# Kernel tuning notes

Hardware: AMD Instinct MI355X
Metric: run time of the kernel (lower is better)

The kernel has to match this reference:

```python
import jax, jax.numpy as jnp
import numpy as np

B, T = 32, 1024
AC, SE, H, NH = 20, 16, 64, 4
HD = H // NH  # 16


def setup_inputs() -> dict:
    key = jax.random.key(0)
    ks = jax.random.split(key, 8)
    g = 0.1  # xavier gain used in _init_weights (rough scale)
    return {
        'acoustic': jax.random.normal(ks[0], (B, T, AC), jnp.float32),
        'semantic': jax.random.normal(ks[1], (B, T, SE), jnp.float32),
        'Wq': jax.random.normal(ks[2], (H, SE), jnp.float32) * g,
        'bq': jnp.zeros((H,), jnp.float32),
        'Wkv': jax.random.normal(ks[3], (2 * H, AC), jnp.float32) * g,
        'bkv': jnp.zeros((2 * H,), jnp.float32),
        'in_w': jax.random.normal(ks[4], (3 * H, H), jnp.float32) * g,
        'in_b': jnp.zeros((3 * H,), jnp.float32),
        'out_w': jax.random.normal(ks[5], (H, H), jnp.float32) * g,
        'out_b': jnp.zeros((H,), jnp.float32),
        'proj_w': jax.random.normal(ks[6], (AC, H), jnp.float32) * g,
        'proj_b': jnp.zeros((AC,), jnp.float32),
        'residual_logit': jnp.float32(-2.0),
        'ln_gamma': jnp.ones((AC,), jnp.float32),
        'ln_beta': jnp.zeros((AC,), jnp.float32),
    }


def _std(x, axis, keepdims=True):
    # torch.std default: unbiased (ddof=1)
    return jnp.std(x, axis=axis, ddof=1, keepdims=keepdims)


def reference(acoustic, semantic, Wq, bq, Wkv, bkv, in_w, in_b, out_w, out_b,
              proj_w, proj_b, residual_logit, ln_gamma, ln_beta):
    # projections to hidden space
    q = semantic @ Wq.T + bq                       # [B,T,H]
    kv = acoustic @ Wkv.T + bkv                    # [B,T,2H]
    k, v = kv[..., :H], kv[..., H:]
    # nn.MultiheadAttention in-projection
    qi = q @ in_w[:H].T + in_b[:H]
    ki = k @ in_w[H:2 * H].T + in_b[H:2 * H]
    vi = v @ in_w[2 * H:].T + in_b[2 * H:]
    # split heads -> [B,T,NH,HD]
    qh = qi.reshape(B, T, NH, HD)
    kh = ki.reshape(B, T, NH, HD)
    vh = vi.reshape(B, T, NH, HD)
    scores = jnp.einsum('bqhd,bkhd->bhqk', qh, kh) / jnp.sqrt(jnp.float32(HD))
    attn = jax.nn.softmax(scores, axis=-1)         # [B,NH,T,T]
    ctx = jnp.einsum('bhqk,bkhd->bqhd', attn, vh).reshape(B, T, H)
    attended = ctx @ out_w.T + out_b               # MHA out_proj
    enhanced_raw = attended @ proj_w.T + proj_b    # [B,T,AC]
    enhanced = acoustic + jax.nn.sigmoid(residual_logit) * enhanced_raw

    # statistics over batch+time (no_grad in torch -> stop_gradient)
    orig_mean = jax.lax.stop_gradient(jnp.mean(acoustic, axis=(0, 1), keepdims=True))
    orig_std = jax.lax.stop_gradient(_std(acoustic, (0, 1)) + 1e-8)
    a_n = (acoustic - orig_mean) / orig_std
    e_n = (enhanced - orig_mean) / orig_std
    std_ratio = _std(e_n, (0, 1)) / (_std(a_n, (0, 1)) + 1e-8)
    std_corr = jnp.where(std_ratio < 0.4, 0.4 / std_ratio, jnp.ones_like(std_ratio))
    enhanced_final = (e_n * std_corr) * orig_std + orig_mean

    # LayerNorm over last dim (biased variance, eps=1e-5)
    mu = jnp.mean(enhanced_final, axis=-1, keepdims=True)
    var = jnp.mean(jnp.square(enhanced_final - mu), axis=-1, keepdims=True)
    return (enhanced_final - mu) * jax.lax.rsqrt(var + 1e-5) * ln_gamma + ln_beta
```

## Files before the change

kernel.cpp:

```cpp
#include <hip/hip_runtime.h>
#include <hip/hip_bf16.h>
#include <math.h>

#define B 32
#define T 1024
#define AC 20
#define SE 16
#define H 64
#define NH 4
#define HD 16
#define NROW (B*T)
#define BH (B*NH)
#define NCHUNK (T/32)
#define NSLOT 128

typedef unsigned short u16;
typedef short short8 __attribute__((ext_vector_type(8)));
typedef float f32x16 __attribute__((ext_vector_type(16)));
typedef unsigned int uintx4 __attribute__((ext_vector_type(4)));

#define F_QB   (BH*T*16/2)
#define OFF_QB   0
#define OFF_KB   (OFF_QB + F_QB)
#define OFF_VT   (OFF_KB + F_QB)
#define OFF_CT   (OFF_VT + F_QB)
#define OFF_ET   (OFF_CT + H*NROW)
#define OFF_WF   (OFF_ET + AC*NROW)
#define OFF_ACC  (OFF_WF + 5120)
#define OFF_ST   (OFF_ACC + NSLOT*80)

#define WF_WQ 0
#define WF_BQ 1024
#define WF_WK 1088
#define WF_BK 2368
#define WF_WV 2432
#define WF_BV 3712
#define WF_WO 3776
#define WF_BO 5056
#define WF_TOTAL 5076

__device__ __forceinline__ u16 bf16b(float a) {
    __hip_bfloat16 t = __float2bfloat16(a);
    u16 u; __builtin_memcpy(&u, &t, 2); return u;
}
__device__ __forceinline__ unsigned packbf(float a, float b) {
    return (unsigned)bf16b(a) | ((unsigned)bf16b(b) << 16);
}

__global__ __launch_bounds__(256) void k_fuse(
    const float* __restrict__ Wq, const float* __restrict__ bq,
    const float* __restrict__ Wkv, const float* __restrict__ bkv,
    const float* __restrict__ in_w, const float* __restrict__ in_b,
    const float* __restrict__ out_w, const float* __restrict__ out_b,
    const float* __restrict__ proj_w, const float* __restrict__ proj_b,
    float* __restrict__ wf, float* __restrict__ accum) {
    int idx = blockIdx.x * 256 + threadIdx.x;
    if (idx < NSLOT*40) {
        accum[idx] = 0.f;
        accum[idx + NSLOT*40] = 0.f;
    }
    if (idx >= WF_TOTAL) return;
    if (idx < WF_BQ) {
        int i = idx >> 4, j = idx & 15;
        float s = 0.f;
        for (int m = 0; m < H; ++m) s += in_w[i*H + m] * Wq[m*SE + j];
        wf[idx] = 0.25f * s;
    } else if (idx < WF_WK) {
        int i = idx - WF_BQ;
        float s = in_b[i];
        for (int m = 0; m < H; ++m) s += in_w[i*H + m] * bq[m];
        wf[idx] = 0.25f * s;
    } else if (idx < WF_BK) {
        int r = idx - WF_WK; int i = r / AC, j = r % AC;
        float s = 0.f;
        for (int m = 0; m < H; ++m) s += in_w[(H+i)*H + m] * Wkv[m*AC + j];
        wf[idx] = s;
    } else if (idx < WF_WV) {
        int i = idx - WF_BK;
        float s = in_b[H + i];
        for (int m = 0; m < H; ++m) s += in_w[(H+i)*H + m] * bkv[m];
        wf[idx] = s;
    } else if (idx < WF_BV) {
        int r = idx - WF_WV; int i = r / AC, j = r % AC;
        float s = 0.f;
        for (int m = 0; m < H; ++m) s += in_w[(2*H+i)*H + m] * Wkv[(H+m)*AC + j];
        wf[idx] = s;
    } else if (idx < WF_WO) {
        int i = idx - WF_BV;
        float s = in_b[2*H + i];
        for (int m = 0; m < H; ++m) s += in_w[(2*H+i)*H + m] * bkv[H + m];
        wf[idx] = s;
    } else if (idx < WF_BO) {
        int r = idx - WF_WO; int c = r >> 6, d = r & 63;
        float s = 0.f;
        for (int m = 0; m < H; ++m) s += proj_w[c*H + m] * out_w[m*H + d];
        wf[idx] = s;
    } else {
        int c = idx - WF_BO;
        float s = proj_b[c];
        for (int m = 0; m < H; ++m) s += proj_w[c*H + m] * out_b[m];
        wf[idx] = s;
    }
}

__global__ __launch_bounds__(192) void k_qkv(
    const float* __restrict__ sem, const float* __restrict__ acst,
    const float* __restrict__ wf,
    u16* __restrict__ Qb, u16* __restrict__ Kb, u16* __restrict__ Vtb) {
    const int tid = threadIdx.x;
    const int sec = tid >> 4, r = tid & 15;
    const int row = blockIdx.x * 16 + r;
    const int b = row >> 10, t = row & 1023;
    const int type = sec >> 2, h = sec & 3;
    float o[16];
    if (type == 0) {
        float s[SE];
        const float4* sp = (const float4*)(sem + (size_t)row * SE);
        #pragma unroll
        for (int i = 0; i < 4; ++i) {
            float4 v = sp[i];
            s[4*i] = v.x; s[4*i+1] = v.y; s[4*i+2] = v.z; s[4*i+3] = v.w;
        }
        const float* wq = wf + WF_WQ + h*16*SE;
        const float* bq = wf + WF_BQ + h*16;
        #pragma unroll
        for (int ii = 0; ii < 16; ++ii) {
            float acc = bq[ii];
            #pragma unroll
            for (int j = 0; j < 4; ++j) {
                float4 w4 = *(const float4*)(wq + ii*SE + 4*j);
                acc += s[4*j]*w4.x + s[4*j+1]*w4.y + s[4*j+2]*w4.z + s[4*j+3]*w4.w;
            }
            o[ii] = acc;
        }
        unsigned* dst = (unsigned*)(Qb + (((size_t)(b*NH + h))*T + t)*16);
        #pragma unroll
        for (int i = 0; i < 8; ++i) dst[i] = packbf(o[2*i], o[2*i+1]);
    } else {
        float a[AC];
        const float4* ap = (const float4*)(acst + (size_t)row * AC);
        #pragma unroll
        for (int i = 0; i < 5; ++i) {
            float4 v = ap[i];
            a[4*i] = v.x; a[4*i+1] = v.y; a[4*i+2] = v.z; a[4*i+3] = v.w;
        }
        const float* wb = wf + (type == 1 ? WF_WK : WF_WV) + h*16*AC;
        const float* bb = wf + (type == 1 ? WF_BK : WF_BV) + h*16;
        #pragma unroll
        for (int ii = 0; ii < 16; ++ii) {
            float acc = bb[ii];
            #pragma unroll
            for (int j = 0; j < 5; ++j) {
                float4 w4 = *(const float4*)(wb + ii*AC + 4*j);
                acc += a[4*j]*w4.x + a[4*j+1]*w4.y + a[4*j+2]*w4.z + a[4*j+3]*w4.w;
            }
            o[ii] = acc;
        }
        if (type == 1) {
            unsigned* dst = (unsigned*)(Kb + (((size_t)(b*NH + h))*T + t)*16);
            #pragma unroll
            for (int i = 0; i < 8; ++i) dst[i] = packbf(o[2*i], o[2*i+1]);
        } else {
            u16* dst = Vtb + ((size_t)(b*NH + h)*64 + (t >> 4))*256 + (t & 15);
            #pragma unroll
            for (int d = 0; d < HD; ++d) dst[d*16] = bf16b(o[d]);
        }
    }
}

__global__ __launch_bounds__(256, 4) void k_attn(
    const u16* __restrict__ Qb, const u16* __restrict__ Kb, const u16* __restrict__ Vtb,
    float* __restrict__ ctxT) {
    const int tid  = threadIdx.x;
    const int lane = tid & 63;
    const int wv   = tid >> 6;
    const int blk  = blockIdx.x;
    const int bh   = blk & 127;
    const int qblk = blk >> 7;
    const int b = bh >> 2, h = bh & 3;
    const int l31 = lane & 31, hi2 = lane >> 5, l15 = lane & 15;
    const int q0 = qblk*128 + wv*32;

    const short8 qf = *(const short8*)(Qb + ((size_t)bh*T + q0 + l31)*16 + 8*hi2);
    const u16* kp = Kb + ((size_t)bh*T + l31)*16 + 8*hi2;
    const u16* vp = Vtb + (size_t)bh*16384 + l15*16 + 8*hi2;

    f32x16 acc = {0.f,0.f,0.f,0.f,0.f,0.f,0.f,0.f,0.f,0.f,0.f,0.f,0.f,0.f,0.f,0.f};
    const f32x16 z16 = {0.f,0.f,0.f,0.f,0.f,0.f,0.f,0.f,0.f,0.f,0.f,0.f,0.f,0.f,0.f,0.f};
    float ls = 0.f;

    short8 kf = *(const short8*)kp;
    short8 va = *(const short8*)vp;
    short8 vb = *(const short8*)(vp + 256);
    #pragma unroll 4
    for (int ch = 0; ch < NCHUNK; ++ch) {
        const int nx = (ch < NCHUNK-1) ? ch + 1 : ch;
        short8 kf_n = *(const short8*)(kp + (size_t)nx*512);
        short8 va_n = *(const short8*)(vp + (size_t)nx*512);
        short8 vb_n = *(const short8*)(vp + (size_t)nx*512 + 256);

        f32x16 sc = __builtin_amdgcn_mfma_f32_32x32x16_bf16(kf, qf, z16, 0, 0, 0);
        float p[16];
        #pragma unroll
        for (int r = 0; r < 16; ++r) p[r] = __expf(sc[r]);
        #pragma unroll
        for (int r = 0; r < 16; ++r) ls += p[r];

        unsigned u0 = packbf(p[0],  p[1]);
        unsigned u1 = packbf(p[2],  p[3]);
        unsigned u2 = packbf(p[4],  p[5]);
        unsigned u3 = packbf(p[6],  p[7]);
        unsigned u4 = packbf(p[8],  p[9]);
        unsigned u5 = packbf(p[10], p[11]);
        unsigned u6 = packbf(p[12], p[13]);
        unsigned u7 = packbf(p[14], p[15]);
        asm("v_permlane32_swap_b32 %0, %1" : "+v"(u2), "+v"(u0));
        asm("v_permlane32_swap_b32 %0, %1" : "+v"(u3), "+v"(u1));
        asm("v_permlane32_swap_b32 %0, %1" : "+v"(u6), "+v"(u4));
        asm("v_permlane32_swap_b32 %0, %1" : "+v"(u7), "+v"(u5));
        uintx4 t1 = {u0, u1, u2, u3};
        uintx4 t2 = {u4, u5, u6, u7};
        short8 pf1 = __builtin_bit_cast(short8, t1);
        short8 pf2 = __builtin_bit_cast(short8, t2);

        acc = __builtin_amdgcn_mfma_f32_32x32x16_bf16(va, pf1, acc, 0, 0, 0);
        acc = __builtin_amdgcn_mfma_f32_32x32x16_bf16(vb, pf2, acc, 0, 0, 0);

        kf = kf_n; va = va_n; vb = vb_n;
    }

    ls += __shfl_xor(ls, 32);
    const float inv = 1.f / ls;
    const int row = b*T + q0 + l31;
    #pragma unroll
    for (int r = 0; r < 8; ++r) {
        const int d = (r & 3) + 8*(r >> 2) + 4*hi2;
        ctxT[(size_t)(h*16 + d)*NROW + row] = acc[r] * inv;
    }
}

#define CSTR 65
__global__ __launch_bounds__(256) void k_proj(
    const float* __restrict__ ctxT, const float* __restrict__ acst,
    const float* __restrict__ wf, const float* __restrict__ rlogit,
    float* __restrict__ enhT, float* __restrict__ accum) {
    __shared__ float ctxs[64*CSTR];
    __shared__ __align__(16) float wsm[AC*H + AC];
    const int tid = threadIdx.x;
    for (int i = tid; i < AC*H + AC; i += 256) wsm[i] = wf[WF_WO + i];
    const int row0 = blockIdx.x * 64;
    for (int i = tid; i < 64*64; i += 256) {
        int ch = i >> 6, rr = i & 63;
        ctxs[rr*CSTR + ch] = ctxT[(size_t)ch*NROW + row0 + rr];
    }
    __syncthreads();
    const int r = tid & 63, cg = tid >> 6;
    const int row = row0 + r;
    float* slot = accum + (size_t)(blockIdx.x & (NSLOT-1)) * 80;
    float c64[H];
    #pragma unroll
    for (int k = 0; k < H; ++k) c64[k] = ctxs[r*CSTR + k];
    float sg = 1.f / (1.f + __expf(-rlogit[0]));
    #pragma unroll
    for (int j = 0; j < 5; ++j) {
        int ch = cg*5 + j;
        float s = wsm[AC*H + ch];
        const float4* w4 = (const float4*)(wsm + ch*H);
        #pragma unroll
        for (int k = 0; k < 16; ++k) {
            float4 w = w4[k];
            s += c64[4*k]*w.x + c64[4*k+1]*w.y + c64[4*k+2]*w.z + c64[4*k+3]*w.w;
        }
        float a = acst[(size_t)row*AC + ch];
        float e = a + sg * s;
        enhT[(size_t)ch * NROW + row] = e;
        float sa = a, qa = a*a, se = e, qe = e*e;
        #pragma unroll
        for (int m = 1; m <= 32; m <<= 1) {
            sa += __shfl_xor(sa, m); qa += __shfl_xor(qa, m);
            se += __shfl_xor(se, m); qe += __shfl_xor(qe, m);
        }
        if (r == 0) {
            atomicAdd(&slot[ch*4+0], sa);
            atomicAdd(&slot[ch*4+1], qa);
            atomicAdd(&slot[ch*4+2], se);
            atomicAdd(&slot[ch*4+3], qe);
        }
    }
}

__global__ __launch_bounds__(640) void k_stats2(
    const float* __restrict__ accum, float* __restrict__ stats) {
    __shared__ float red[80*8];
    __shared__ float acs[80];
    const int tx = threadIdx.x;
    const int c = tx >> 3, p = tx & 7;
    float s0 = 0.f, s1 = 0.f, s2 = 0.f, s3 = 0.f;
    #pragma unroll
    for (int i = 0; i < 4; ++i) {
        int sl = p + (4*i)*8;
        s0 += accum[(size_t)sl*80 + c];
        s1 += accum[(size_t)(sl+8)*80 + c];
        s2 += accum[(size_t)(sl+16)*80 + c];
        s3 += accum[(size_t)(sl+24)*80 + c];
    }
    red[c*8 + p] = (s0 + s1) + (s2 + s3);
    __syncthreads();
    if (tx < 80) {
        float t = 0.f;
        #pragma unroll
        for (int i = 0; i < 8; ++i) t += red[tx*8 + i];
        acs[tx] = t;
    }
    __syncthreads();
    if (tx < AC) {
        const float Nf = (float)NROW;
        float sa = acs[tx*4+0], qa = acs[tx*4+1];
        float se = acs[tx*4+2], qe = acs[tx*4+3];
        float mu  = sa / Nf;
        float va  = (qa - sa*sa/Nf) / (Nf - 1.f);
        float sda = sqrtf(fmaxf(va, 0.f));
        float osd = sda + 1e-8f;
        float ve  = (qe - se*se/Nf) / (Nf - 1.f);
        float sde = sqrtf(fmaxf(ve, 0.f));
        float ratio = (sde / osd) / (sda / osd + 1e-8f);
        float corr  = (ratio < 0.4f) ? (0.4f / ratio) : 1.f;
        stats[tx*2]   = mu;
        stats[tx*2+1] = corr;
    }
}

__global__ __launch_bounds__(128) void k_final(
    const float* __restrict__ enhT, const float* __restrict__ stats,
    const float* __restrict__ gamma, const float* __restrict__ beta,
    float* __restrict__ out) {
    __shared__ float acs[40];
    const int tx = threadIdx.x;
    if (tx < 40) acs[tx] = stats[tx];
    __syncthreads();
    int row = blockIdx.x * 128 + tx;
    float ef[AC];
    #pragma unroll
    for (int c = 0; c < AC; ++c) {
        float mu = acs[c*2], corr = acs[c*2+1];
        float e = enhT[(size_t)c * NROW + row];
        ef[c] = (e - mu) * corr + mu;
    }
    float m = 0.f;
    #pragma unroll
    for (int c = 0; c < AC; ++c) m += ef[c];
    m *= (1.f / AC);
    float v = 0.f;
    #pragma unroll
    for (int c = 0; c < AC; ++c) { float d = ef[c] - m; v += d*d; }
    v *= (1.f / AC);
    float inv = rsqrtf(v + 1e-5f);
    float o[AC];
    #pragma unroll
    for (int c = 0; c < AC; ++c) o[c] = (ef[c] - m) * inv * gamma[c] + beta[c];
    float4* op = (float4*)(out + (size_t)row * AC);
    #pragma unroll
    for (int i = 0; i < 5; ++i)
        op[i] = make_float4(o[4*i], o[4*i+1], o[4*i+2], o[4*i+3]);
}

extern "C" void kernel_launch(void* const* d_in, const int* in_sizes, int n_in,
                              void* d_out, int out_size, void* d_ws, size_t ws_size,
                              hipStream_t stream) {
    (void)in_sizes; (void)n_in; (void)out_size; (void)ws_size;
    const float* acoustic = (const float*)d_in[0];
    const float* semantic = (const float*)d_in[1];
    const float* Wq     = (const float*)d_in[2];
    const float* bq     = (const float*)d_in[3];
    const float* Wkv    = (const float*)d_in[4];
    const float* bkv    = (const float*)d_in[5];
    const float* in_w   = (const float*)d_in[6];
    const float* in_b   = (const float*)d_in[7];
    const float* out_w  = (const float*)d_in[8];
    const float* out_b  = (const float*)d_in[9];
    const float* proj_w = (const float*)d_in[10];
    const float* proj_b = (const float*)d_in[11];
    const float* rlogit = (const float*)d_in[12];
    const float* gamma  = (const float*)d_in[13];
    const float* beta   = (const float*)d_in[14];
    float* ws = (float*)d_ws;
    u16* Qb  = (u16*)(ws + OFF_QB);
    u16* Kb  = (u16*)(ws + OFF_KB);
    u16* Vtb = (u16*)(ws + OFF_VT);
    float* ctxT  = ws + OFF_CT;
    float* enhT  = ws + OFF_ET;
    float* wf    = ws + OFF_WF;
    float* accum = ws + OFF_ACC;
    float* stats = ws + OFF_ST;
    float* out = (float*)d_out;

    k_fuse<<<(WF_TOTAL + 255)/256, 256, 0, stream>>>(Wq, bq, Wkv, bkv, in_w, in_b,
                                                     out_w, out_b, proj_w, proj_b, wf, accum);
    k_qkv<<<NROW/16, 192, 0, stream>>>(semantic, acoustic, wf, Qb, Kb, Vtb);
    k_attn<<<8*BH, 256, 0, stream>>>(Qb, Kb, Vtb, ctxT);
    k_proj<<<NROW/64, 256, 0, stream>>>(ctxT, acoustic, wf, rlogit, enhT, accum);
    k_stats2<<<1, 640, 0, stream>>>(accum, stats);
    k_final<<<NROW/128, 128, 0, stream>>>(enhT, stats, gamma, beta, out);
}
```

Baseline: 159.3 us.

## Fuse output projection and statistics into attention kernel, drop ctx buffer

The attention kernel's block mapping changes so each block covers all four heads of one batch for 32 query rows, with one wave per head. The per-head context goes into shared memory, and the same block then applies the fused out/proj weights, the residual sigmoid blend and the per-channel sum/sumsq atomics. This removes the separate k_proj launch and the global round trip of the 64-channel ctxT buffer. In exchange each block does serial projection work after its attention loop, adds about 13 KB of shared memory per block, and has fewer query rows per head per block.

Result: faster. 151.7 us (-4.8%).

```diff
diff --git a/kernel.cpp b/kernel.cpp
--- a/kernel.cpp
+++ b/kernel.cpp
@@ -23,8 +23,7 @@
 #define OFF_QB   0
 #define OFF_KB   (OFF_QB + F_QB)
 #define OFF_VT   (OFF_KB + F_QB)
-#define OFF_CT   (OFF_VT + F_QB)
-#define OFF_ET   (OFF_CT + H*NROW)
+#define OFF_ET   (OFF_VT + F_QB)
 #define OFF_WF   (OFF_ET + AC*NROW)
 #define OFF_ACC  (OFF_WF + 5120)
 #define OFF_ST   (OFF_ACC + NSLOT*80)
@@ -168,18 +167,24 @@
     }
 }
 
+#define CSTR 66
 __global__ __launch_bounds__(256, 4) void k_attn(
     const u16* __restrict__ Qb, const u16* __restrict__ Kb, const u16* __restrict__ Vtb,
-    float* __restrict__ ctxT) {
+    const float* __restrict__ acst, const float* __restrict__ wf,
+    const float* __restrict__ rlogit,
+    float* __restrict__ enhT, float* __restrict__ accum) {
+    __shared__ __align__(16) float ctxs[32*CSTR];
+    __shared__ __align__(16) float wsm[AC*H + AC];
     const int tid  = threadIdx.x;
     const int lane = tid & 63;
     const int wv   = tid >> 6;
+    for (int i = tid; i < AC*H + AC; i += 256) wsm[i] = wf[WF_WO + i];
     const int blk  = blockIdx.x;
-    const int bh   = blk & 127;
-    const int qblk = blk >> 7;
-    const int b = bh >> 2, h = bh & 3;
+    const int b    = blk & 31;
+    const int qblk = blk >> 5;
     const int l31 = lane & 31, hi2 = lane >> 5, l15 = lane & 15;
-    const int q0 = qblk*128 + wv*32;
+    const int bh = b*NH + wv;
+    const int q0 = qblk*32;
 
     const short8 qf = *(const short8*)(Qb + ((size_t)bh*T + q0 + l31)*16 + 8*hi2);
     const u16* kp = Kb + ((size_t)bh*T + l31)*16 + 8*hi2;
@@ -231,56 +236,47 @@
 
     ls += __shfl_xor(ls, 32);
     const float inv = 1.f / ls;
-    const int row = b*T + q0 + l31;
     #pragma unroll
     for (int r = 0; r < 8; ++r) {
         const int d = (r & 3) + 8*(r >> 2) + 4*hi2;
-        ctxT[(size_t)(h*16 + d)*NROW + row] = acc[r] * inv;
-    }
-}
-
-#define CSTR 65
-__global__ __launch_bounds__(256) void k_proj(
-    const float* __restrict__ ctxT, const float* __restrict__ acst,
-    const float* __restrict__ wf, const float* __restrict__ rlogit,
-    float* __restrict__ enhT, float* __restrict__ accum) {
-    __shared__ float ctxs[64*CSTR];
-    __shared__ __align__(16) float wsm[AC*H + AC];
-    const int tid = threadIdx.x;
-    for (int i = tid; i < AC*H + AC; i += 256) wsm[i] = wf[WF_WO + i];
-    const int row0 = blockIdx.x * 64;
-    for (int i = tid; i < 64*64; i += 256) {
-        int ch = i >> 6, rr = i & 63;
-        ctxs[rr*CSTR + ch] = ctxT[(size_t)ch*NROW + row0 + rr];
+        ctxs[l31*CSTR + wv*16 + d] = acc[r] * inv;
     }
     __syncthreads();
-    const int r = tid & 63, cg = tid >> 6;
-    const int row = row0 + r;
-    float* slot = accum + (size_t)(blockIdx.x & (NSLOT-1)) * 80;
-    float c64[H];
-    #pragma unroll
-    for (int k = 0; k < H; ++k) c64[k] = ctxs[r*CSTR + k];
-    float sg = 1.f / (1.f + __expf(-rlogit[0]));
-    #pragma unroll
-    for (int j = 0; j < 5; ++j) {
-        int ch = cg*5 + j;
+
+    const int rq = tid & 31, g = tid >> 5;
+    const int row = b*T + q0 + rq;
+    const float sg = 1.f / (1.f + __expf(-rlogit[0]));
+    float* slot = accum + (size_t)(blk & (NSLOT-1)) * 80;
+    const int nj = (g < 4) ? 3 : 2;
+    for (int j = 0; j < nj; ++j) {
+        const int ch = g + 8*j;
         float s = wsm[AC*H + ch];
-        const float4* w4 = (const float4*)(wsm + ch*H);
-        #pragma unroll
-        for (int k = 0; k < 16; ++k) {
-            float4 w = w4[k];
-            s += c64[4*k]*w.x + c64[4*k+1]*w.y + c64[4*k+2]*w.z + c64[4*k+3]*w.w;
-        }
-        float a = acst[(size_t)row*AC + ch];
-        float e = a + sg * s;
+        #pragma unroll
+        for (int kc = 0; kc < 4; ++kc) {
+            float c0 = ctxs[rq*CSTR + kc*16 +  0], c1 = ctxs[rq*CSTR + kc*16 +  1];
+            float c2 = ctxs[rq*CSTR + kc*16 +  2], c3 = ctxs[rq*CSTR + kc*16 +  3];
+            float c4 = ctxs[rq*CSTR + kc*16 +  4], c5 = ctxs[rq*CSTR + kc*16 +  5];
+            float c6 = ctxs[rq*CSTR + kc*16 +  6], c7 = ctxs[rq*CSTR + kc*16 +  7];
+            float c8 = ctxs[rq*CSTR + kc*16 +  8], c9 = ctxs[rq*CSTR + kc*16 +  9];
+            float cA = ctxs[rq*CSTR + kc*16 + 10], cB = ctxs[rq*CSTR + kc*16 + 11];
+            float cC = ctxs[rq*CSTR + kc*16 + 12], cD = ctxs[rq*CSTR + kc*16 + 13];
+            float cE = ctxs[rq*CSTR + kc*16 + 14], cF = ctxs[rq*CSTR + kc*16 + 15];
+            const float* w = wsm + ch*H + kc*16;
+            s += c0*w[0] + c1*w[1] + c2*w[2] + c3*w[3]
+               + c4*w[4] + c5*w[5] + c6*w[6] + c7*w[7]
+               + c8*w[8] + c9*w[9] + cA*w[10] + cB*w[11]
+               + cC*w[12] + cD*w[13] + cE*w[14] + cF*w[15];
+        }
+        const float a = acst[(size_t)row*AC + ch];
+        const float e = a + sg * s;
         enhT[(size_t)ch * NROW + row] = e;
         float sa = a, qa = a*a, se = e, qe = e*e;
         #pragma unroll
-        for (int m = 1; m <= 32; m <<= 1) {
+        for (int m = 1; m <= 16; m <<= 1) {
             sa += __shfl_xor(sa, m); qa += __shfl_xor(qa, m);
             se += __shfl_xor(se, m); qe += __shfl_xor(qe, m);
         }
-        if (r == 0) {
+        if (rq == 0) {
             atomicAdd(&slot[ch*4+0], sa);
             atomicAdd(&slot[ch*4+1], qa);
             atomicAdd(&slot[ch*4+2], se);
@@ -387,7 +383,6 @@
     u16* Qb  = (u16*)(ws + OFF_QB);
     u16* Kb  = (u16*)(ws + OFF_KB);
     u16* Vtb = (u16*)(ws + OFF_VT);
-    float* ctxT  = ws + OFF_CT;
     float* enhT  = ws + OFF_ET;
     float* wf    = ws + OFF_WF;
     float* accum = ws + OFF_ACC;
@@ -397,8 +392,7 @@
     k_fuse<<<(WF_TOTAL + 255)/256, 256, 0, stream>>>(Wq, bq, Wkv, bkv, in_w, in_b,
                                                      out_w, out_b, proj_w, proj_b, wf, accum);
     k_qkv<<<NROW/16, 192, 0, stream>>>(semantic, acoustic, wf, Qb, Kb, Vtb);
-    k_attn<<<8*BH, 256, 0, stream>>>(Qb, Kb, Vtb, ctxT);
-    k_proj<<<NROW/64, 256, 0, stream>>>(ctxT, acoustic, wf, rlogit, enhT, accum);
+    k_attn<<<1024, 256, 0, stream>>>(Qb, Kb, Vtb, acoustic, wf, rlogit, enhT, accum);
     k_stats2<<<1, 640, 0, stream>>>(accum, stats);
     k_final<<<NROW/128, 128, 0, stream>>>(enhT, stats, gamma, beta, out);
 }
```
